# Performance work log

Measured on AMD Instinct MI355X. Metric: run time of the kernel, lower is better.

The kernel has to match this reference:

```python
import jax, jax.numpy as jnp
import numpy as np

B, N, C, H = 4, 1024, 512, 8
HD = C // H
SCALE = HD ** -0.5
LN_EPS = 1e-5


def setup_inputs() -> dict:
    key = jax.random.key(0)
    ks = jax.random.split(key, 4)
    return {
        "x": jax.random.normal(ks[0], (B, N, C), dtype=jnp.float32),
        "Wqkv": jax.random.normal(ks[1], (C, 3 * C), dtype=jnp.float32) * (C ** -0.5),
        "bqkv": jnp.zeros((3 * C,), dtype=jnp.float32),
        "order_weights": jnp.ones((3,), dtype=jnp.float32),
        "Wproj": jax.random.normal(ks[2], (C, C), dtype=jnp.float32) * (C ** -0.5),
        "bproj": jnp.zeros((C,), dtype=jnp.float32),
        "gamma": jnp.ones((C,), dtype=jnp.float32),
        "beta": jnp.zeros((C,), dtype=jnp.float32),
    }


def reference(x, Wqkv, bqkv, order_weights, Wproj, bproj, gamma, beta):
    b, n, c = x.shape
    qkv = (x @ Wqkv + bqkv).reshape(b, n, 3, H, HD)
    qkv = jnp.transpose(qkv, (2, 0, 3, 1, 4))  # [3, B, H, N, HD]
    q, k, v = qkv[0], qkv[1], qkv[2]

    base = jnp.einsum('bhnd,bhmd->bhnm', q, k) * SCALE  # [B, H, N, N]

    ow = jax.nn.softmax(order_weights)
    # torch loop: term_0 = base, term_i = base**(i+1)
    attn = ow[0] * base
    cur = base
    for i in range(1, order_weights.shape[0]):
        cur = cur * base
        attn = attn + ow[i] * cur

    attn_final = jax.nn.softmax(attn, axis=-1)

    out = jnp.einsum('bhnm,bhmd->bhnd', attn_final, v)
    out = jnp.transpose(out, (0, 2, 1, 3)).reshape(b, n, c)
    out = out @ Wproj + bproj

    y = x + out
    mu = jnp.mean(y, axis=-1, keepdims=True)
    var = jnp.var(y, axis=-1, keepdims=True)
    y = (y - mu) / jnp.sqrt(var + LN_EPS) * gamma + beta
    return y, attn_final
```

## Files before the change

kernel.cpp:

```cpp
#include <hip/hip_runtime.h>
#include <math.h>

#define B_ 4
#define N_ 1024
#define C_ 512
#define H_ 8
#define HD_ 64
#define SCALE_ 0.125f
#define LN_EPS_ 1e-5f

__global__ __launch_bounds__(256) void qkv_gemm(const float* __restrict__ x,
                                                const float* __restrict__ Wqkv,
                                                const float* __restrict__ bqkv,
                                                float* __restrict__ qkv) {
    const int K = C_;
    const int NN = 3 * C_;
    __shared__ float As[64][17];
    __shared__ float Bs[16][64];

    const int tid = threadIdx.x;
    const int tx = tid & 15;
    const int ty = tid >> 4;
    const int row0 = blockIdx.y * 64;
    const int col0 = blockIdx.x * 64;

    float acc[4][4] = {};

    for (int kt = 0; kt < K; kt += 16) {
        {
            int lin = tid * 4;
            int m = lin >> 4;
            int k = lin & 15;
            float4 a = *(const float4*)&x[(size_t)(row0 + m) * K + kt + k];
            As[m][k + 0] = a.x; As[m][k + 1] = a.y;
            As[m][k + 2] = a.z; As[m][k + 3] = a.w;
        }
        {
            int lin = tid * 4;
            int kk = lin >> 6;
            int n = lin & 63;
            *(float4*)&Bs[kk][n] =
                *(const float4*)&Wqkv[(size_t)(kt + kk) * NN + col0 + n];
        }
        __syncthreads();
#pragma unroll
        for (int kk = 0; kk < 16; ++kk) {
            float a[4], bb[4];
#pragma unroll
            for (int i = 0; i < 4; ++i) a[i] = As[ty * 4 + i][kk];
#pragma unroll
            for (int j = 0; j < 4; ++j) bb[j] = Bs[kk][tx * 4 + j];
#pragma unroll
            for (int i = 0; i < 4; ++i)
#pragma unroll
                for (int j = 0; j < 4; ++j) acc[i][j] += a[i] * bb[j];
        }
        __syncthreads();
    }
#pragma unroll
    for (int i = 0; i < 4; ++i) {
        int r = row0 + ty * 4 + i;
        int c = col0 + tx * 4;
        float4 o;
        o.x = acc[i][0] + bqkv[c + 0];
        o.y = acc[i][1] + bqkv[c + 1];
        o.z = acc[i][2] + bqkv[c + 2];
        o.w = acc[i][3] + bqkv[c + 3];
        *(float4*)&qkv[(size_t)r * NN + c] = o;
    }
}

__global__ __launch_bounds__(256) void attn_scores(const float* __restrict__ qkv,
                                                   const float* __restrict__ ow_in,
                                                   float* __restrict__ attn) {
    __shared__ __align__(16) float Qst[64][20];
    __shared__ __align__(16) float Kst[16][264];

    const int tid = threadIdx.x;
    const int lane = tid & 63;
    const int ry = tid >> 6;
    const int n0 = blockIdx.x * 16;
    const int bh = blockIdx.y;
    const int b = bh >> 3, h = bh & 7;
    const size_t RS = 3 * C_;

    float w0 = ow_in[0], w1 = ow_in[1], w2 = ow_in[2];
    float wm = fmaxf(w0, fmaxf(w1, w2));
    float e0 = __expf(w0 - wm), e1 = __expf(w1 - wm), e2 = __expf(w2 - wm);
    float einv = 1.0f / (e0 + e1 + e2);
    float ow0 = e0 * einv, ow1 = e1 * einv, ow2 = e2 * einv;

    {
        int r = tid >> 4, f = tid & 15;
        const float* qrow = qkv + (size_t)(b * N_ + n0 + r) * RS + h * HD_;
        float4 qv = ((const float4*)qrow)[f];
        Qst[f * 4 + 0][r] = qv.x; Qst[f * 4 + 1][r] = qv.y;
        Qst[f * 4 + 2][r] = qv.z; Qst[f * 4 + 3][r] = qv.w;
    }

    float s[4][16];
    float lmax[4] = {-1e30f, -1e30f, -1e30f, -1e30f};

#pragma unroll
    for (int ct = 0; ct < 4; ++ct) {
#pragma unroll
        for (int u = 0; u < 16; ++u) s[ct][u] = 0.f;
#pragma unroll
        for (int kc = 0; kc < 4; ++kc) {
            const float* krow =
                qkv + (size_t)(b * N_ + ct * 256 + tid) * RS + C_ + h * HD_ + kc * 16;
            float4 kv0 = ((const float4*)krow)[0];
            float4 kv1 = ((const float4*)krow)[1];
            float4 kv2 = ((const float4*)krow)[2];
            float4 kv3 = ((const float4*)krow)[3];
            __syncthreads();
            Kst[ 0][tid] = kv0.x; Kst[ 1][tid] = kv0.y; Kst[ 2][tid] = kv0.z; Kst[ 3][tid] = kv0.w;
            Kst[ 4][tid] = kv1.x; Kst[ 5][tid] = kv1.y; Kst[ 6][tid] = kv1.z; Kst[ 7][tid] = kv1.w;
            Kst[ 8][tid] = kv2.x; Kst[ 9][tid] = kv2.y; Kst[10][tid] = kv2.z; Kst[11][tid] = kv2.w;
            Kst[12][tid] = kv3.x; Kst[13][tid] = kv3.y; Kst[14][tid] = kv3.z; Kst[15][tid] = kv3.w;
            __syncthreads();
#pragma unroll
            for (int kk = 0; kk < 16; ++kk) {
                float4 a4 = *(const float4*)&Qst[kc * 16 + kk][ry * 4];
                float4 b4 = *(const float4*)&Kst[kk][lane * 4];
                float a[4] = {a4.x, a4.y, a4.z, a4.w};
                float bb[4] = {b4.x, b4.y, b4.z, b4.w};
#pragma unroll
                for (int i = 0; i < 4; ++i)
#pragma unroll
                    for (int jj = 0; jj < 4; ++jj)
                        s[ct][i * 4 + jj] += a[i] * bb[jj];
            }
        }
#pragma unroll
        for (int i = 0; i < 4; ++i)
#pragma unroll
            for (int jj = 0; jj < 4; ++jj) {
                float sc = s[ct][i * 4 + jj] * SCALE_;
                float l = sc * (ow0 + sc * (ow1 + sc * ow2));
                s[ct][i * 4 + jj] = l;
                lmax[i] = fmaxf(lmax[i], l);
            }
    }

#pragma unroll
    for (int i = 0; i < 4; ++i)
#pragma unroll
        for (int m = 1; m < 64; m <<= 1)
            lmax[i] = fmaxf(lmax[i], __shfl_xor(lmax[i], m, 64));

    float lsum[4] = {0.f, 0.f, 0.f, 0.f};
#pragma unroll
    for (int ct = 0; ct < 4; ++ct)
#pragma unroll
        for (int i = 0; i < 4; ++i)
#pragma unroll
            for (int jj = 0; jj < 4; ++jj) {
                float e = __expf(s[ct][i * 4 + jj] - lmax[i]);
                s[ct][i * 4 + jj] = e;
                lsum[i] += e;
            }
#pragma unroll
    for (int i = 0; i < 4; ++i)
#pragma unroll
        for (int m = 1; m < 64; m <<= 1)
            lsum[i] += __shfl_xor(lsum[i], m, 64);

    float inv[4];
#pragma unroll
    for (int i = 0; i < 4; ++i) inv[i] = 1.0f / lsum[i];

#pragma unroll
    for (int ct = 0; ct < 4; ++ct)
#pragma unroll
        for (int i = 0; i < 4; ++i) {
            float4 p;
            p.x = s[ct][i * 4 + 0] * inv[i];
            p.y = s[ct][i * 4 + 1] * inv[i];
            p.z = s[ct][i * 4 + 2] * inv[i];
            p.w = s[ct][i * 4 + 3] * inv[i];
            *(float4*)&attn[((size_t)bh * N_ + n0 + ry * 4 + i) * N_ + ct * 256 + lane * 4] = p;
        }
}

__global__ __launch_bounds__(256) void pv_gemm(const float* __restrict__ qkv,
                                               const float* __restrict__ attn,
                                               float* __restrict__ ctx) {
    __shared__ __align__(16) float Pst[64][68];
    __shared__ __align__(16) float Vs[64][68];

    const int tid = threadIdx.x;
    const int tx = tid & 15;
    const int ty = tid >> 4;
    const int n0 = blockIdx.x * 64;
    const int bh = blockIdx.y;
    const int b = bh >> 3, h = bh & 7;
    const size_t RS = 3 * C_;

    const int rr = tid >> 2;
    const int q = tid & 3;

    float acc[4][4] = {};

    for (int mt = 0; mt < 16; ++mt) {
        const int m0 = mt * 64;
        const float* prow = attn + ((size_t)bh * N_ + n0 + rr) * N_ + m0 + q * 16;
        const float* vrow = qkv + (size_t)(b * N_ + m0 + rr) * RS + 2 * C_ + h * HD_ + q * 16;
        float4 pv[4], vv[4];
#pragma unroll
        for (int m = 0; m < 4; ++m) pv[m] = ((const float4*)prow)[m];
#pragma unroll
        for (int m = 0; m < 4; ++m) vv[m] = ((const float4*)vrow)[m];
        __syncthreads();
#pragma unroll
        for (int m = 0; m < 4; ++m) {
            int c = q * 16 + m * 4;
            Pst[c + 0][rr] = pv[m].x; Pst[c + 1][rr] = pv[m].y;
            Pst[c + 2][rr] = pv[m].z; Pst[c + 3][rr] = pv[m].w;
            *(float4*)&Vs[rr][c] = vv[m];
        }
        __syncthreads();
#pragma unroll 16
        for (int mm = 0; mm < 64; ++mm) {
            float4 a4 = *(const float4*)&Pst[mm][ty * 4];
            float4 b4 = *(const float4*)&Vs[mm][tx * 4];
            float a[4] = {a4.x, a4.y, a4.z, a4.w};
            float bb[4] = {b4.x, b4.y, b4.z, b4.w};
#pragma unroll
            for (int i = 0; i < 4; ++i)
#pragma unroll
                for (int j = 0; j < 4; ++j) acc[i][j] += a[i] * bb[j];
        }
    }
#pragma unroll
    for (int i = 0; i < 4; ++i) {
        float4 o;
        o.x = acc[i][0]; o.y = acc[i][1]; o.z = acc[i][2]; o.w = acc[i][3];
        *(float4*)&ctx[(size_t)(b * N_ + n0 + ty * 4 + i) * C_ + h * HD_ + tx * 4] = o;
    }
}

__global__ __launch_bounds__(256) void proj_gemm(const float* __restrict__ ctx,
                                                 const float* __restrict__ x,
                                                 const float* __restrict__ Wproj,
                                                 const float* __restrict__ bproj,
                                                 float* __restrict__ y) {
    const int K = C_;
    const int NN = C_;
    __shared__ float As[64][17];
    __shared__ float Bs[16][64];

    const int tid = threadIdx.x;
    const int tx = tid & 15;
    const int ty = tid >> 4;
    const int row0 = blockIdx.y * 64;
    const int col0 = blockIdx.x * 64;

    float acc[4][4] = {};

    for (int kt = 0; kt < K; kt += 16) {
        {
            int lin = tid * 4;
            int m = lin >> 4;
            int k = lin & 15;
            float4 a = *(const float4*)&ctx[(size_t)(row0 + m) * K + kt + k];
            As[m][k + 0] = a.x; As[m][k + 1] = a.y;
            As[m][k + 2] = a.z; As[m][k + 3] = a.w;
        }
        {
            int lin = tid * 4;
            int kk = lin >> 6;
            int n = lin & 63;
            *(float4*)&Bs[kk][n] =
                *(const float4*)&Wproj[(size_t)(kt + kk) * NN + col0 + n];
        }
        __syncthreads();
#pragma unroll
        for (int kk = 0; kk < 16; ++kk) {
            float a[4], bb[4];
#pragma unroll
            for (int i = 0; i < 4; ++i) a[i] = As[ty * 4 + i][kk];
#pragma unroll
            for (int j = 0; j < 4; ++j) bb[j] = Bs[kk][tx * 4 + j];
#pragma unroll
            for (int i = 0; i < 4; ++i)
#pragma unroll
                for (int j = 0; j < 4; ++j) acc[i][j] += a[i] * bb[j];
        }
        __syncthreads();
    }
#pragma unroll
    for (int i = 0; i < 4; ++i) {
        int r = row0 + ty * 4 + i;
        int c = col0 + tx * 4;
        float4 xr = *(const float4*)&x[(size_t)r * C_ + c];
        float4 o;
        o.x = acc[i][0] + bproj[c + 0] + xr.x;
        o.y = acc[i][1] + bproj[c + 1] + xr.y;
        o.z = acc[i][2] + bproj[c + 2] + xr.z;
        o.w = acc[i][3] + bproj[c + 3] + xr.w;
        *(float4*)&y[(size_t)r * C_ + c] = o;
    }
}

__global__ __launch_bounds__(256) void ln_kernel(float* __restrict__ y,
                                                 const float* __restrict__ gamma,
                                                 const float* __restrict__ beta) {
    __shared__ float wsum[4], wsq[4];
    const int row = blockIdx.x;
    const int tid = threadIdx.x;
    const int lane = tid & 63;
    const int w = tid >> 6;

    float2 v = ((const float2*)(y + (size_t)row * C_))[tid];
    float s = v.x + v.y;
    float sq = v.x * v.x + v.y * v.y;
#pragma unroll
    for (int m = 1; m < 64; m <<= 1) {
        s += __shfl_xor(s, m, 64);
        sq += __shfl_xor(sq, m, 64);
    }
    if (lane == 0) { wsum[w] = s; wsq[w] = sq; }
    __syncthreads();
    float ts = wsum[0] + wsum[1] + wsum[2] + wsum[3];
    float tq = wsq[0] + wsq[1] + wsq[2] + wsq[3];
    float mu = ts * (1.0f / C_);
    float var = tq * (1.0f / C_) - mu * mu;
    float rstd = rsqrtf(var + LN_EPS_);

    float2 g = ((const float2*)gamma)[tid];
    float2 be = ((const float2*)beta)[tid];
    float2 o;
    o.x = (v.x - mu) * rstd * g.x + be.x;
    o.y = (v.y - mu) * rstd * g.y + be.y;
    ((float2*)(y + (size_t)row * C_))[tid] = o;
}

extern "C" void kernel_launch(void* const* d_in, const int* in_sizes, int n_in,
                              void* d_out, int out_size, void* d_ws, size_t ws_size,
                              hipStream_t stream) {
    const float* x     = (const float*)d_in[0];
    const float* Wqkv  = (const float*)d_in[1];
    const float* bqkv  = (const float*)d_in[2];
    const float* ow    = (const float*)d_in[3];
    const float* Wproj = (const float*)d_in[4];
    const float* bproj = (const float*)d_in[5];
    const float* gamma = (const float*)d_in[6];
    const float* beta  = (const float*)d_in[7];

    float* out  = (float*)d_out;
    float* y    = out;
    float* attn = out + (size_t)B_ * N_ * C_;
    float* qkv  = (float*)d_ws;
    float* ctx  = qkv + (size_t)B_ * N_ * 3 * C_;

    dim3 g1(3 * C_ / 64, B_ * N_ / 64);
    qkv_gemm<<<g1, 256, 0, stream>>>(x, Wqkv, bqkv, qkv);

    dim3 g2(N_ / 16, B_ * H_);
    attn_scores<<<g2, 256, 0, stream>>>(qkv, ow, attn);

    dim3 g3(N_ / 64, B_ * H_);
    pv_gemm<<<g3, 256, 0, stream>>>(qkv, attn, ctx);

    dim3 g4(C_ / 64, B_ * N_ / 64);
    proj_gemm<<<g4, 256, 0, stream>>>(ctx, x, Wproj, bproj, y);

    ln_kernel<<<B_ * N_, 256, 0, stream>>>(y, gamma, beta);
}
```

Before: 463.7 us.

## Use split-bf16 MFMA for QKV GEMM and restructure score kernel without K staging

```diff
diff --git a/kernel.cpp b/kernel.cpp
--- a/kernel.cpp
+++ b/kernel.cpp
@@ -9,64 +9,119 @@
 #define SCALE_ 0.125f
 #define LN_EPS_ 1e-5f
 
-__global__ __launch_bounds__(256) void qkv_gemm(const float* __restrict__ x,
-                                                const float* __restrict__ Wqkv,
-                                                const float* __restrict__ bqkv,
-                                                float* __restrict__ qkv) {
-    const int K = C_;
-    const int NN = 3 * C_;
-    __shared__ float As[64][17];
-    __shared__ float Bs[16][64];
+typedef short bf16x8 __attribute__((ext_vector_type(8)));
+typedef float f32x4 __attribute__((ext_vector_type(4)));
+
+__device__ __forceinline__ void split_store16(unsigned short* __restrict__ Hh,
+                                              unsigned short* __restrict__ Hl,
+                                              int srow, int khalf,
+                                              const float* __restrict__ f) {
+    uint hp[8], lp[8];
+#pragma unroll
+    for (int i = 0; i < 8; ++i) {
+        uint u0 = __float_as_uint(f[2 * i]);
+        uint u1 = __float_as_uint(f[2 * i + 1]);
+        uint h0 = u0 & 0xffff0000u;
+        uint h1 = u1 & 0xffff0000u;
+        float lo0 = f[2 * i]     - __uint_as_float(h0);
+        float lo1 = f[2 * i + 1] - __uint_as_float(h1);
+        hp[i] = (u0 >> 16) | (u1 & 0xffff0000u);
+        lp[i] = (__float_as_uint(lo0) >> 16) | (__float_as_uint(lo1) & 0xffff0000u);
+    }
+    uint4* dh = (uint4*)&Hh[srow * 32 + khalf * 16];
+    dh[0] = make_uint4(hp[0], hp[1], hp[2], hp[3]);
+    dh[1] = make_uint4(hp[4], hp[5], hp[6], hp[7]);
+    uint4* dl = (uint4*)&Hl[srow * 32 + khalf * 16];
+    dl[0] = make_uint4(lp[0], lp[1], lp[2], lp[3]);
+    dl[1] = make_uint4(lp[4], lp[5], lp[6], lp[7]);
+}
+
+__global__ __launch_bounds__(256) void qkv_gemm_mfma(const float* __restrict__ x,
+                                                     const float* __restrict__ Wqkv,
+                                                     const float* __restrict__ bqkv,
+                                                     float* __restrict__ qkv) {
+    __shared__ __align__(16) unsigned short Ah[128 * 32];
+    __shared__ __align__(16) unsigned short Al[128 * 32];
+    __shared__ __align__(16) unsigned short Bh[128 * 32];
+    __shared__ __align__(16) unsigned short Bl[128 * 32];
 
     const int tid = threadIdx.x;
-    const int tx = tid & 15;
-    const int ty = tid >> 4;
-    const int row0 = blockIdx.y * 64;
-    const int col0 = blockIdx.x * 64;
-
-    float acc[4][4] = {};
-
-    for (int kt = 0; kt < K; kt += 16) {
+    const int lane = tid & 63;
+    const int wv = tid >> 6;
+    const int wm = wv & 1, wn = wv >> 1;
+    const int quad = lane >> 4, l15 = lane & 15;
+    const int row0 = blockIdx.y * 128;
+    const int col0 = blockIdx.x * 128;
+    const int sr = tid >> 1;
+    const int kh = tid & 1;
+
+    f32x4 acc[4][4];
+#pragma unroll
+    for (int mt = 0; mt < 4; ++mt)
+#pragma unroll
+        for (int nt = 0; nt < 4; ++nt)
+            acc[mt][nt] = (f32x4){0.f, 0.f, 0.f, 0.f};
+
+    for (int kt = 0; kt < 512; kt += 32) {
+        float a[16];
         {
-            int lin = tid * 4;
-            int m = lin >> 4;
-            int k = lin & 15;
-            float4 a = *(const float4*)&x[(size_t)(row0 + m) * K + kt + k];
-            As[m][k + 0] = a.x; As[m][k + 1] = a.y;
-            As[m][k + 2] = a.z; As[m][k + 3] = a.w;
-        }
+            const float* ap = x + (size_t)(row0 + sr) * 512 + kt + kh * 16;
+#pragma unroll
+            for (int j = 0; j < 4; ++j) {
+                float4 v = ((const float4*)ap)[j];
+                a[j * 4 + 0] = v.x; a[j * 4 + 1] = v.y;
+                a[j * 4 + 2] = v.z; a[j * 4 + 3] = v.w;
+            }
+        }
+        float w[16];
         {
-            int lin = tid * 4;
-            int kk = lin >> 6;
-            int n = lin & 63;
-            *(float4*)&Bs[kk][n] =
-                *(const float4*)&Wqkv[(size_t)(kt + kk) * NN + col0 + n];
-        }
-        __syncthreads();
-#pragma unroll
-        for (int kk = 0; kk < 16; ++kk) {
-            float a[4], bb[4];
-#pragma unroll
-            for (int i = 0; i < 4; ++i) a[i] = As[ty * 4 + i][kk];
-#pragma unroll
-            for (int j = 0; j < 4; ++j) bb[j] = Bs[kk][tx * 4 + j];
-#pragma unroll
-            for (int i = 0; i < 4; ++i)
-#pragma unroll
-                for (int j = 0; j < 4; ++j) acc[i][j] += a[i] * bb[j];
-        }
-        __syncthreads();
-    }
-#pragma unroll
-    for (int i = 0; i < 4; ++i) {
-        int r = row0 + ty * 4 + i;
-        int c = col0 + tx * 4;
-        float4 o;
-        o.x = acc[i][0] + bqkv[c + 0];
-        o.y = acc[i][1] + bqkv[c + 1];
-        o.z = acc[i][2] + bqkv[c + 2];
-        o.w = acc[i][3] + bqkv[c + 3];
-        *(float4*)&qkv[(size_t)r * NN + c] = o;
+            const float* bp = Wqkv + (size_t)(kt + kh * 16) * 1536 + col0 + sr;
+#pragma unroll
+            for (int kk = 0; kk < 16; ++kk) w[kk] = bp[(size_t)kk * 1536];
+        }
+        __syncthreads();
+        split_store16(Ah, Al, sr, kh, a);
+        split_store16(Bh, Bl, sr, kh, w);
+        __syncthreads();
+
+        bf16x8 ah[4], al4[4], bh4[4], bl4[4];
+#pragma unroll
+        for (int mt = 0; mt < 4; ++mt) {
+            int base = (wm * 64 + mt * 16 + l15) * 32 + quad * 8;
+            ah[mt]  = *(const bf16x8*)&Ah[base];
+            al4[mt] = *(const bf16x8*)&Al[base];
+        }
+#pragma unroll
+        for (int nt = 0; nt < 4; ++nt) {
+            int base = (wn * 64 + nt * 16 + l15) * 32 + quad * 8;
+            bh4[nt] = *(const bf16x8*)&Bh[base];
+            bl4[nt] = *(const bf16x8*)&Bl[base];
+        }
+#pragma unroll
+        for (int mt = 0; mt < 4; ++mt)
+#pragma unroll
+            for (int nt = 0; nt < 4; ++nt) {
+                acc[mt][nt] = __builtin_amdgcn_mfma_f32_16x16x32_bf16(
+                    ah[mt], bh4[nt], acc[mt][nt], 0, 0, 0);
+                acc[mt][nt] = __builtin_amdgcn_mfma_f32_16x16x32_bf16(
+                    ah[mt], bl4[nt], acc[mt][nt], 0, 0, 0);
+                acc[mt][nt] = __builtin_amdgcn_mfma_f32_16x16x32_bf16(
+                    al4[mt], bh4[nt], acc[mt][nt], 0, 0, 0);
+            }
+    }
+
+#pragma unroll
+    for (int nt = 0; nt < 4; ++nt) {
+        int cg = col0 + wn * 64 + nt * 16 + l15;
+        float bias = bqkv[cg];
+#pragma unroll
+        for (int mt = 0; mt < 4; ++mt) {
+#pragma unroll
+            for (int r = 0; r < 4; ++r) {
+                int rg = row0 + wm * 64 + mt * 16 + quad * 4 + r;
+                qkv[(size_t)rg * 1536 + cg] = acc[mt][nt][r] + bias;
+            }
+        }
     }
 }
 
@@ -74,11 +129,11 @@
                                                    const float* __restrict__ ow_in,
                                                    float* __restrict__ attn) {
     __shared__ __align__(16) float Qst[64][20];
-    __shared__ __align__(16) float Kst[16][264];
+    __shared__ float wred[16][5];
 
     const int tid = threadIdx.x;
     const int lane = tid & 63;
-    const int ry = tid >> 6;
+    const int wv = tid >> 6;
     const int n0 = blockIdx.x * 16;
     const int bh = blockIdx.y;
     const int b = bh >> 3, h = bh & 7;
@@ -97,90 +152,106 @@
         Qst[f * 4 + 0][r] = qv.x; Qst[f * 4 + 1][r] = qv.y;
         Qst[f * 4 + 2][r] = qv.z; Qst[f * 4 + 3][r] = qv.w;
     }
+    __syncthreads();
 
     float s[4][16];
-    float lmax[4] = {-1e30f, -1e30f, -1e30f, -1e30f};
-
-#pragma unroll
-    for (int ct = 0; ct < 4; ++ct) {
-#pragma unroll
-        for (int u = 0; u < 16; ++u) s[ct][u] = 0.f;
-#pragma unroll
-        for (int kc = 0; kc < 4; ++kc) {
-            const float* krow =
-                qkv + (size_t)(b * N_ + ct * 256 + tid) * RS + C_ + h * HD_ + kc * 16;
-            float4 kv0 = ((const float4*)krow)[0];
-            float4 kv1 = ((const float4*)krow)[1];
-            float4 kv2 = ((const float4*)krow)[2];
-            float4 kv3 = ((const float4*)krow)[3];
-            __syncthreads();
-            Kst[ 0][tid] = kv0.x; Kst[ 1][tid] = kv0.y; Kst[ 2][tid] = kv0.z; Kst[ 3][tid] = kv0.w;
-            Kst[ 4][tid] = kv1.x; Kst[ 5][tid] = kv1.y; Kst[ 6][tid] = kv1.z; Kst[ 7][tid] = kv1.w;
-            Kst[ 8][tid] = kv2.x; Kst[ 9][tid] = kv2.y; Kst[10][tid] = kv2.z; Kst[11][tid] = kv2.w;
-            Kst[12][tid] = kv3.x; Kst[13][tid] = kv3.y; Kst[14][tid] = kv3.z; Kst[15][tid] = kv3.w;
-            __syncthreads();
-#pragma unroll
-            for (int kk = 0; kk < 16; ++kk) {
-                float4 a4 = *(const float4*)&Qst[kc * 16 + kk][ry * 4];
-                float4 b4 = *(const float4*)&Kst[kk][lane * 4];
-                float a[4] = {a4.x, a4.y, a4.z, a4.w};
-                float bb[4] = {b4.x, b4.y, b4.z, b4.w};
-#pragma unroll
-                for (int i = 0; i < 4; ++i)
-#pragma unroll
-                    for (int jj = 0; jj < 4; ++jj)
-                        s[ct][i * 4 + jj] += a[i] * bb[jj];
+#pragma unroll
+    for (int u = 0; u < 4; ++u)
+#pragma unroll
+        for (int r = 0; r < 16; ++r) s[u][r] = 0.f;
+
+    const float* kbase = qkv + (size_t)(b * N_) * RS + C_ + h * HD_;
+
+    for (int k4 = 0; k4 < 16; ++k4) {
+        float4 kv[4];
+#pragma unroll
+        for (int u = 0; u < 4; ++u)
+            kv[u] = *(const float4*)(kbase + (size_t)(u * 256 + tid) * RS + k4 * 4);
+#pragma unroll
+        for (int kk = 0; kk < 4; ++kk) {
+            float4 a0 = *(const float4*)&Qst[k4 * 4 + kk][0];
+            float4 a1 = *(const float4*)&Qst[k4 * 4 + kk][4];
+            float4 a2 = *(const float4*)&Qst[k4 * 4 + kk][8];
+            float4 a3 = *(const float4*)&Qst[k4 * 4 + kk][12];
+#pragma unroll
+            for (int u = 0; u < 4; ++u) {
+                const float* kvf = (const float*)&kv[u];
+                float bv = kvf[kk];
+                s[u][0]  += a0.x * bv; s[u][1]  += a0.y * bv;
+                s[u][2]  += a0.z * bv; s[u][3]  += a0.w * bv;
+                s[u][4]  += a1.x * bv; s[u][5]  += a1.y * bv;
+                s[u][6]  += a1.z * bv; s[u][7]  += a1.w * bv;
+                s[u][8]  += a2.x * bv; s[u][9]  += a2.y * bv;
+                s[u][10] += a2.z * bv; s[u][11] += a2.w * bv;
+                s[u][12] += a3.x * bv; s[u][13] += a3.y * bv;
+                s[u][14] += a3.z * bv; s[u][15] += a3.w * bv;
             }
         }
-#pragma unroll
-        for (int i = 0; i < 4; ++i)
-#pragma unroll
-            for (int jj = 0; jj < 4; ++jj) {
-                float sc = s[ct][i * 4 + jj] * SCALE_;
-                float l = sc * (ow0 + sc * (ow1 + sc * ow2));
-                s[ct][i * 4 + jj] = l;
-                lmax[i] = fmaxf(lmax[i], l);
-            }
-    }
-
-#pragma unroll
-    for (int i = 0; i < 4; ++i)
+    }
+
+    float pm[16];
+#pragma unroll
+    for (int r = 0; r < 16; ++r) pm[r] = -1e30f;
+#pragma unroll
+    for (int u = 0; u < 4; ++u)
+#pragma unroll
+        for (int r = 0; r < 16; ++r) {
+            float sc = s[u][r] * SCALE_;
+            float l = sc * (ow0 + sc * (ow1 + sc * ow2));
+            s[u][r] = l;
+            pm[r] = fmaxf(pm[r], l);
+        }
+
+#pragma unroll
+    for (int r = 0; r < 16; ++r)
 #pragma unroll
         for (int m = 1; m < 64; m <<= 1)
-            lmax[i] = fmaxf(lmax[i], __shfl_xor(lmax[i], m, 64));
-
-    float lsum[4] = {0.f, 0.f, 0.f, 0.f};
-#pragma unroll
-    for (int ct = 0; ct < 4; ++ct)
-#pragma unroll
-        for (int i = 0; i < 4; ++i)
-#pragma unroll
-            for (int jj = 0; jj < 4; ++jj) {
-                float e = __expf(s[ct][i * 4 + jj] - lmax[i]);
-                s[ct][i * 4 + jj] = e;
-                lsum[i] += e;
-            }
-#pragma unroll
-    for (int i = 0; i < 4; ++i)
+            pm[r] = fmaxf(pm[r], __shfl_xor(pm[r], m, 64));
+    if (lane == 0) {
+#pragma unroll
+        for (int r = 0; r < 16; ++r) wred[r][wv] = pm[r];
+    }
+    __syncthreads();
+    float rowmax[16];
+#pragma unroll
+    for (int r = 0; r < 16; ++r)
+        rowmax[r] = fmaxf(fmaxf(wred[r][0], wred[r][1]),
+                          fmaxf(wred[r][2], wred[r][3]));
+
+    float ps[16];
+#pragma unroll
+    for (int r = 0; r < 16; ++r) ps[r] = 0.f;
+#pragma unroll
+    for (int u = 0; u < 4; ++u)
+#pragma unroll
+        for (int r = 0; r < 16; ++r) {
+            float e = __expf(s[u][r] - rowmax[r]);
+            s[u][r] = e;
+            ps[r] += e;
+        }
+    __syncthreads();
+#pragma unroll
+    for (int r = 0; r < 16; ++r)
 #pragma unroll
         for (int m = 1; m < 64; m <<= 1)
-            lsum[i] += __shfl_xor(lsum[i], m, 64);
-
-    float inv[4];
-#pragma unroll
-    for (int i = 0; i < 4; ++i) inv[i] = 1.0f / lsum[i];
-
-#pragma unroll
-    for (int ct = 0; ct < 4; ++ct)
-#pragma unroll
-        for (int i = 0; i < 4; ++i) {
-            float4 p;
-            p.x = s[ct][i * 4 + 0] * inv[i];
-            p.y = s[ct][i * 4 + 1] * inv[i];
-            p.z = s[ct][i * 4 + 2] * inv[i];
-            p.w = s[ct][i * 4 + 3] * inv[i];
-            *(float4*)&attn[((size_t)bh * N_ + n0 + ry * 4 + i) * N_ + ct * 256 + lane * 4] = p;
-        }
+            ps[r] += __shfl_xor(ps[r], m, 64);
+    if (lane == 0) {
+#pragma unroll
+        for (int r = 0; r < 16; ++r) wred[r][wv] = ps[r];
+    }
+    __syncthreads();
+    float inv[16];
+#pragma unroll
+    for (int r = 0; r < 16; ++r)
+        inv[r] = 1.0f / (wred[r][0] + wred[r][1] + wred[r][2] + wred[r][3]);
+
+#pragma unroll
+    for (int r = 0; r < 16; ++r) {
+        float* orow = attn + ((size_t)bh * N_ + n0 + r) * N_;
+#pragma unroll
+        for (int u = 0; u < 4; ++u)
+            orow[u * 256 + tid] = s[u][r] * inv[r];
+    }
 }
 
 __global__ __launch_bounds__(256) void pv_gemm(const float* __restrict__ qkv,
@@ -354,8 +425,8 @@
     float* qkv  = (float*)d_ws;
     float* ctx  = qkv + (size_t)B_ * N_ * 3 * C_;
 
-    dim3 g1(3 * C_ / 64, B_ * N_ / 64);
-    qkv_gemm<<<g1, 256, 0, stream>>>(x, Wqkv, bqkv, qkv);
+    dim3 g1(3 * C_ / 128, B_ * N_ / 128);
+    qkv_gemm_mfma<<<g1, 256, 0, stream>>>(x, Wqkv, bqkv, qkv);
 
     dim3 g2(N_ / 16, B_ * H_);
     attn_scores<<<g2, 256, 0, stream>>>(qkv, ow, attn);
```

Result: no change. 470.6 us (+1.5%).
